# Performance work log

Measured on AMD Instinct MI355X. Metric: run time of the kernel, lower is better.

Reference implementation:

```python
import jax, jax.numpy as jnp
import numpy as np

B, N, F_IN, F_HID, F_EMB, H, L_DIM = 8, 1024, 128, 128, 128, 8, 2


def _xavier(key, shape, fan_in, fan_out):
    lim = np.sqrt(6.0 / (fan_in + fan_out))
    return jax.random.uniform(key, shape, jnp.float32, -lim, lim)


def setup_inputs() -> dict:
    key = jax.random.key(0)
    ks = jax.random.split(key, 16)
    x = jax.random.normal(ks[0], (B, N, F_IN), jnp.float32)
    # sparse 0/1 adjacency with self loops (avoids fully-masked softmax rows)
    adj = (jax.random.uniform(ks[1], (B, N, N)) < 0.05).astype(jnp.float32)
    adj = jnp.maximum(adj, jnp.eye(N, dtype=jnp.float32)[None])
    def gat_params(k, f_in, f_out):
        k1, k2, k3 = jax.random.split(k, 3)
        return (_xavier(k1, (H, f_in, f_out), f_in, f_out),
                _xavier(k2, (H, f_out, 1), f_out, 1),
                _xavier(k3, (H, f_out, 1), f_out, 1),
                jnp.zeros((f_out,), jnp.float32))
    w1, as1, ad1, b1 = gat_params(ks[2], F_IN, F_HID)
    w2, as2, ad2, b2 = gat_params(ks[3], F_HID, F_HID)
    w3, as3, ad3, b3 = gat_params(ks[4], F_HID, F_EMB)
    pred_in = F_HID * 2 + F_EMB  # hidden*(num_layers-1)+embedding, concat=True
    pw = _xavier(ks[5], (pred_in, L_DIM), pred_in, L_DIM)
    pb = jnp.zeros((L_DIM,), jnp.float32)
    return {"x": x, "adj": adj,
            "w1": w1, "as1": as1, "ad1": ad1, "b1": b1,
            "w2": w2, "as2": as2, "ad2": ad2, "b2": b2,
            "w3": w3, "as3": as3, "ad3": ad3, "b3": b3,
            "pw": pw, "pb": pb}


def gat_layer(h, adj, w, a_src, a_dst, bias):
    # h: [B,N,f_in] -> h_prime: [B,H,N,f_out]
    hp = jnp.einsum('bnf,hfo->bhno', h, w)
    t = jnp.tanh(hp)
    s = jnp.einsum('bhno,hoi->bhni', t, a_src)[..., 0]  # [B,H,N]
    d = jnp.einsum('bhno,hoi->bhni', t, a_dst)[..., 0]  # [B,H,N]
    scores = s[:, :, :, None] + d[:, :, None, :]        # [B,H,N,N]
    scores = jnp.where(scores >= 0, scores, 0.2 * scores)  # LeakyReLU(0.2)
    scores = jnp.where(adj[:, None, :, :] > 0, scores, -jnp.inf)
    attn = jax.nn.softmax(scores, axis=-1)  # dropout disabled (eval mode)
    out = jnp.einsum('bhnm,bhmo->bhno', attn, hp) + bias
    return out.mean(axis=1)  # merge heads -> [B,N,f_out]


def reference(x, adj, w1, as1, ad1, b1, w2, as2, ad2, b2, w3, as3, ad3, b3, pw, pb):
    x1 = jax.nn.relu(gat_layer(x, adj, w1, as1, ad1, b1))
    x2 = jax.nn.relu(gat_layer(x1, adj, w2, as2, ad2, b2))
    x3 = gat_layer(x2, adj, w3, as3, ad3, b3)
    x_all = jnp.concatenate([x1, x2, x3], axis=2)  # [B,N,pred_in]
    pooled = jnp.max(x_all, axis=1)                # max over nodes -> [B,pred_in]
    return pooled @ pw + pb                        # [B,label_dim]
```

## Files before the change

kernel.cpp:

```cpp
#include <hip/hip_runtime.h>
#include <hip/hip_fp16.h>

#define BB 8
#define NN 1024
#define FF 128
#define HH 8

typedef _Float16 f16;
typedef f16  f16x8 __attribute__((ext_vector_type(8)));
typedef f16  f16x4 __attribute__((ext_vector_type(4)));
typedef float f32x4 __attribute__((ext_vector_type(4)));

#define L2E 1.44269504f

__global__ void k_pre(const float* __restrict__ x, f16* __restrict__ x16a,
                      const float* __restrict__ w1, const float* __restrict__ w2,
                      const float* __restrict__ w3, f16* __restrict__ wB,
                      const float* __restrict__ adj, unsigned* __restrict__ am){
  int bid = blockIdx.x, t = threadIdx.x;
  if (bid < 512){
    int i = (bid*256 + t)*8;
    float4 a = *(const float4*)(x+i), b = *(const float4*)(x+i+4);
    f16x8 v;
    v[0]=(f16)a.x; v[1]=(f16)a.y; v[2]=(f16)a.z; v[3]=(f16)a.w;
    v[4]=(f16)b.x; v[5]=(f16)b.y; v[6]=(f16)b.z; v[7]=(f16)b.w;
    *(f16x8*)(x16a+i) = v;
  } else if (bid < 704){
    int e = (bid-512)*256 + t;
    int fc = e & 15, c = (e>>4)&127, h = (e>>11)&7, l = e>>14;
    const float* w = (l==0) ? w1 : ((l==1) ? w2 : w3);
    f16x8 v;
    #pragma unroll
    for(int j=0;j<8;j++) v[j] = (f16)w[(h*128 + fc*8 + j)*128 + c];
    *(f16x8*)(wB + (((l*8+h)*16 + fc)*128 + c)*8) = v;
  } else {
    int wv = t >> 6, lane = t & 63;
    int r = (bid-704)*4 + wv;
    const float* row = adj + (long)r*1024;
    for(int g=0; g<16; g++){
      float v = row[g*64 + lane];
      unsigned long long mb = __ballot(v > 0.0f);
      if (lane == 0){
        am[r*32 + 2*g]   = (unsigned)mb;
        am[r*32 + 2*g+1] = (unsigned)(mb >> 32);
      }
    }
  }
}

__global__ __launch_bounds__(256,2) void k_hp(
    const f16* __restrict__ xin,
    const f16* __restrict__ wBl,
    const float* __restrict__ asrc, const float* __restrict__ adst,
    f16* __restrict__ hpB,
    float* __restrict__ sarr, float* __restrict__ darr)
{
  __shared__ f16 xs[128*136];
  __shared__ float asl[128], adl[128];
  int t = threadIdx.x;
  int bid = blockIdx.x;
  int it = bid & 7, h = (bid>>3)&7, b = bid>>6;
  int i0 = it*128;
  {
    const f16* src = xin + (long)(b*1024 + i0)*128;
    int fc = t & 15, r0 = t >> 4;
    #pragma unroll
    for(int p=0;p<8;p++){
      int r = r0 + p*16;
      f16x8 v = *(const f16x8*)(src + r*128 + fc*8);
      *(f16x8*)(xs + r*136 + fc*8) = v;
    }
  }
  if (t < 128){ asl[t] = asrc[h*128+t]; adl[t] = adst[h*128+t]; }
  __syncthreads();

  int lane = t & 63, wv = t>>6, wr = wv>>1, wc = wv&1;
  int mq = lane & 15, quad = lane >> 4;
  f32x4 acc[4][4];
  #pragma unroll
  for(int a=0;a<4;a++)
    #pragma unroll
    for(int c=0;c<4;c++) acc[a][c] = (f32x4){0.f,0.f,0.f,0.f};

  const f16* wh = wBl + h*16*128*8;
  #pragma unroll
  for(int ks=0; ks<4; ks++){
    f16x8 af[4], bf[4];
    #pragma unroll
    for(int mt=0; mt<4; mt++)
      af[mt] = *(const f16x8*)(xs + (wr*64 + mt*16 + mq)*136 + ks*32 + quad*8);
    #pragma unroll
    for(int nt=0; nt<4; nt++){
      int c  = wc*64 + nt*16 + mq;
      int fc = ks*4 + quad;
      bf[nt] = *(const f16x8*)(wh + (fc*128 + c)*8);
    }
    #pragma unroll
    for(int mt=0; mt<4; mt++)
      #pragma unroll
      for(int nt=0; nt<4; nt++)
        acc[mt][nt] = __builtin_amdgcn_mfma_f32_16x16x32_f16(af[mt], bf[nt], acc[mt][nt], 0,0,0);
  }
  __syncthreads();
  f16* tt = xs;
  f16* hpb = hpB + (long)(b*8+h)*128*128*8;
  #pragma unroll
  for(int mt=0; mt<4; mt++){
    #pragma unroll
    for(int nt=0; nt<4; nt++){
      int c = wc*64 + nt*16 + mq;
      f16x4 pk;
      #pragma unroll
      for(int rg=0; rg<4; rg++){
        float v = acc[mt][nt][rg];
        pk[rg] = (f16)v;
        int il = wr*64 + mt*16 + quad*4 + rg;
        float e2 = __expf(2.0f*v);
        float th = 1.0f - 2.0f*__builtin_amdgcn_rcpf(e2 + 1.0f);
        tt[il*136 + c] = (f16)th;
      }
      int il0 = wr*64 + mt*16 + quad*4;
      int inode = i0 + il0;
      *(f16x4*)(hpb + ((long)(inode>>3)*128 + c)*8 + (inode&7)) = pk;
    }
  }
  __syncthreads();
  {
    int r = t>>1, hf = t&1;
    float s_p = 0.f, d_p = 0.f;
    #pragma unroll
    for(int q=0;q<8;q++){
      f16x8 tv = *(const f16x8*)(tt + r*136 + hf*64 + q*8);
      #pragma unroll
      for(int j=0;j<8;j++){
        float tvf = (float)tv[j];
        int c = hf*64 + q*8 + j;
        s_p = fmaf(tvf, asl[c], s_p);
        d_p = fmaf(tvf, adl[c], d_p);
      }
    }
    s_p += __shfl_xor(s_p, 1);
    d_p += __shfl_xor(d_p, 1);
    if (hf == 0){
      sarr[(b*8+h)*1024 + i0 + r] = s_p;
      darr[(b*8+h)*1024 + i0 + r] = d_p;
    }
  }
}

__global__ __launch_bounds__(256,4) void k_attn(
    const f16* __restrict__ hpB,
    const float* __restrict__ sarr, const float* __restrict__ darr,
    const unsigned* __restrict__ am,
    f16* __restrict__ part,
    float* __restrict__ zpart)
{
  __shared__ float ddl[512];
  __shared__ float wred[4];
  __shared__ f16 Pl[2][128*40];
  int t = threadIdx.x;
  int bid = blockIdx.x;
  int bh = bid & 63, q = bid >> 6;
  int jh = q & 1, it = q >> 1;
  int i0 = it*128, j0 = jh*512;
  int b = bh >> 3;

  {
    float4 v = *(const float4*)(darr + bh*1024 + t*4);
    float mx = fmaxf(fmaxf(v.x,v.y), fmaxf(v.z,v.w));
    #pragma unroll
    for(int o=1;o<64;o<<=1) mx = fmaxf(mx, __shfl_xor(mx, o));
    if ((t&63)==0) wred[t>>6] = mx;
    int base = t*4 - j0;
    if (base >= 0 && base < 512){
      float4 s = make_float4(v.x*L2E, v.y*L2E, v.z*L2E, v.w*L2E);
      *(float4*)(ddl + base) = s;
    }
  }
  __syncthreads();
  float Dml = fmaxf(fmaxf(wred[0],wred[1]), fmaxf(wred[2],wred[3])) * L2E;

  int prow = t>>1, pjg = t&1;
  float srowl = sarr[bh*1024 + i0 + prow] * L2E;
  float ml = srowl + Dml;
  float mrowl = fmaxf(ml, 0.2f*ml);
  const unsigned* amrow = am + ((long)(b*1024 + i0 + prow))*32 + jh*16;

  int lane = t&63, wv = t>>6, wr = wv>>1, wc = wv&1;
  int mq = lane&15, quad = lane>>4;
  const f16* hpb = hpB + (long)bh*128*128*8;
  f32x4 acc[4][4];
  #pragma unroll
  for(int a=0;a<4;a++)
    #pragma unroll
    for(int c=0;c<4;c++) acc[a][c] = (f32x4){0.f,0.f,0.f,0.f};
  float zacc = 0.f;
  f16x8 zerov = (f16x8){0,0,0,0,0,0,0,0};

  f16* myp0 = Pl[0] + prow*40 + pjg*16;
  f16* myp1 = Pl[1] + prow*40 + pjg*16;

  auto compP = [&](int jtn, f16* myp){
    *(f16x8*)(myp)     = zerov;
    *(f16x8*)(myp + 8) = zerov;
    unsigned word = (amrow[jtn] >> (pjg*16)) & 0xffffu;
    const float* dloc = ddl + jtn*32 + pjg*16;
    while(word){
      int j = __builtin_ctz(word);
      word &= word - 1u;
      float xl  = srowl + dloc[j];
      float scl = fmaxf(xl, 0.2f*xl);
      float e   = __builtin_amdgcn_exp2f(scl - mrowl);
      zacc += e;
      myp[j] = (f16)e;
    }
  };

  compP(0, myp0);

  #pragma unroll 2
  for(int jt=0; jt<16; jt++){
    f16x8 bf[4];
    #pragma unroll
    for(int nt=0;nt<4;nt++){
      int c  = wc*64 + nt*16 + mq;
      int jc = jh*64 + jt*4 + quad;
      bf[nt] = *(const f16x8*)(hpb + (jc*128 + c)*8);
    }
    __syncthreads();
    const f16* Pb = Pl[jt&1];
    f16x8 af[4];
    #pragma unroll
    for(int mt=0;mt<4;mt++)
      af[mt] = *(const f16x8*)(Pb + (wr*64 + mt*16 + mq)*40 + quad*8);
    if (jt < 15) compP(jt+1, ((jt+1)&1) ? myp1 : myp0);
    #pragma unroll
    for(int mt=0;mt<4;mt++)
      #pragma unroll
      for(int nt=0;nt<4;nt++)
        acc[mt][nt] = __builtin_amdgcn_mfma_f32_16x16x32_f16(af[mt], bf[nt], acc[mt][nt], 0,0,0);
  }
  zacc += __shfl_xor(zacc, 1);
  if (pjg == 0) zpart[(jh*64 + bh)*1024 + i0 + prow] = zacc;
  f16* pout = part + ((long)(jh*64 + bh)*1024 + i0)*128;
  #pragma unroll
  for(int mt=0;mt<4;mt++){
    #pragma unroll
    for(int nt=0;nt<4;nt++){
      int c = wc*64 + nt*16 + mq;
      #pragma unroll
      for(int rg=0;rg<4;rg++){
        int il = wr*64 + mt*16 + quad*4 + rg;
        pout[il*128 + c] = (f16)acc[mt][nt][rg];
      }
    }
  }
}

__global__ void k_fin(const f16* __restrict__ part, const float* __restrict__ zp,
                      const float* __restrict__ bias,
                      f16* __restrict__ x16, float* __restrict__ pmax, int do_relu){
  __shared__ float pm[16][128];
  int t = threadIdx.x;
  int idx = blockIdx.x*256 + t;
  int c8 = idx & 15, n = (idx>>4)&1023, b = idx>>14;
  float s[8];
  #pragma unroll
  for(int j=0;j<8;j++) s[j] = 0.f;
  #pragma unroll
  for(int h=0;h<8;h++){
    int bh = b*8 + h;
    float zi = 0.125f / (zp[bh*1024 + n] + zp[65536 + bh*1024 + n]);
    f16x8 p0 = *(const f16x8*)(part + ((long)bh*1024 + n)*128 + c8*8);
    f16x8 p1 = *(const f16x8*)(part + ((long)(64+bh)*1024 + n)*128 + c8*8);
    #pragma unroll
    for(int j=0;j<8;j++) s[j] = fmaf((float)p0[j] + (float)p1[j], zi, s[j]);
  }
  f16x8 h8;
  float ov[8];
  #pragma unroll
  for(int j=0;j<8;j++){
    float v = s[j] + bias[c8*8 + j];
    if (do_relu) v = fmaxf(v, 0.f);
    ov[j] = v;
    h8[j] = (f16)v;
  }
  if (x16) *(f16x8*)(x16 + ((long)(b*1024+n))*128 + c8*8) = h8;
  #pragma unroll
  for(int j=0;j<8;j++) pm[n&15][c8*8+j] = ov[j];
  __syncthreads();
  if (t < 128){
    float m = pm[0][t];
    #pragma unroll
    for(int r=1;r<16;r++) m = fmaxf(m, pm[r][t]);
    pmax[blockIdx.x*128 + t] = m;
  }
}

__global__ void k_pool2(const float* __restrict__ pmax, const float* __restrict__ pw,
                        const float* __restrict__ pb, float* __restrict__ out){
  __shared__ float pl[384];
  int b = blockIdx.x, t = threadIdx.x;
  for(int f = t; f < 384; f += 256){
    int l = f >> 7, c = f & 127;
    const float* p = pmax + l*65536 + b*64*128 + c;
    float mx = -3.4e38f;
    #pragma unroll 8
    for(int k=0;k<64;k++) mx = fmaxf(mx, p[k*128]);
    pl[f] = mx;
  }
  __syncthreads();
  if (t < 64){
    float a0 = 0.f, a1 = 0.f;
    #pragma unroll
    for(int k=0;k<6;k++){
      int f = t + 64*k;
      float v = pl[f];
      a0 = fmaf(v, pw[f*2],   a0);
      a1 = fmaf(v, pw[f*2+1], a1);
    }
    #pragma unroll
    for(int o=1;o<64;o<<=1){ a0 += __shfl_xor(a0,o); a1 += __shfl_xor(a1,o); }
    if (t == 0){ out[b*2] = a0 + pb[0]; out[b*2+1] = a1 + pb[1]; }
  }
}

extern "C" void kernel_launch(void* const* d_in, const int* in_sizes, int n_in,
                              void* d_out, int out_size, void* d_ws, size_t ws_size,
                              hipStream_t stream) {
  const float* x   = (const float*)d_in[0];
  const float* adj = (const float*)d_in[1];
  const float* w1  = (const float*)d_in[2];
  const float* as1 = (const float*)d_in[3];
  const float* ad1 = (const float*)d_in[4];
  const float* b1  = (const float*)d_in[5];
  const float* w2  = (const float*)d_in[6];
  const float* as2 = (const float*)d_in[7];
  const float* ad2 = (const float*)d_in[8];
  const float* b2  = (const float*)d_in[9];
  const float* w3  = (const float*)d_in[10];
  const float* as3 = (const float*)d_in[11];
  const float* ad3 = (const float*)d_in[12];
  const float* b3  = (const float*)d_in[13];
  const float* pw  = (const float*)d_in[14];
  const float* pb  = (const float*)d_in[15];

  char* ws = (char*)d_ws;
  f16*      x16a = (f16*)ws;                 ws += (size_t)1048576*2;
  f16*      x16b = (f16*)ws;                 ws += (size_t)1048576*2;
  f16*      wB   = (f16*)ws;                 ws += (size_t)393216*2;
  unsigned* am   = (unsigned*)ws;            ws += (size_t)8*1024*32*4;
  f16*      hpB  = (f16*)ws;                 ws += (size_t)8*8*1024*128*2;
  float*    sarr = (float*)ws;               ws += (size_t)65536*4;
  float*    darr = (float*)ws;               ws += (size_t)65536*4;
  f16*      part = (f16*)ws;                 ws += (size_t)2*64*1024*128*2;
  float*    zp   = (float*)ws;               ws += (size_t)2*65536*4;
  float*    pmax = (float*)ws;               ws += (size_t)3*512*128*4;

  k_pre<<<2752, 256, 0, stream>>>(x, x16a, w1, w2, w3, wB, adj, am);

  k_hp  <<<512, 256, 0, stream>>>(x16a, wB,            as1, ad1, hpB, sarr, darr);
  k_attn<<<1024,256, 0, stream>>>(hpB, sarr, darr, am, part, zp);
  k_fin <<<512, 256, 0, stream>>>(part, zp, b1, x16b, pmax,           1);
  k_hp  <<<512, 256, 0, stream>>>(x16b, wB + 131072,   as2, ad2, hpB, sarr, darr);
  k_attn<<<1024,256, 0, stream>>>(hpB, sarr, darr, am, part, zp);
  k_fin <<<512, 256, 0, stream>>>(part, zp, b2, x16a, pmax + 65536,   1);
  k_hp  <<<512, 256, 0, stream>>>(x16a, wB + 262144,   as3, ad3, hpB, sarr, darr);
  k_attn<<<1024,256, 0, stream>>>(hpB, sarr, darr, am, part, zp);
  k_fin <<<512, 256, 0, stream>>>(part, zp, b3, nullptr, pmax + 131072, 0);

  k_pool2<<<8, 256, 0, stream>>>(pmax, pw, pb, (float*)d_out);
}
```

Baseline: 260.0 us.

## Compute attention P tiles branch-free with vectorized loads and prefetched mask words

The sparse per-bit loop (ctz over mask bits with scattered LDS writes plus zeroing) is replaced by a dense, fully unrolled computation of all 16 exponentials, masked with a select and stored as two f16x8 vectors. Adjacency mask words are now prefetched two iterations ahead to hide global load latency. The adjacency read in the mask-building kernel also switches to a nontemporal load. The dense form removes divergent control flow, but it computes exponentials for every entry even though the mask is about 5% dense.

```diff
diff --git a/kernel.cpp b/kernel.cpp
--- a/kernel.cpp
+++ b/kernel.cpp
@@ -38,7 +38,7 @@
     int r = (bid-704)*4 + wv;
     const float* row = adj + (long)r*1024;
     for(int g=0; g<16; g++){
-      float v = row[g*64 + lane];
+      float v = __builtin_nontemporal_load(row + g*64 + lane);
       unsigned long long mb = __ballot(v > 0.0f);
       if (lane == 0){
         am[r*32 + 2*g]   = (unsigned)mb;
@@ -49,11 +49,9 @@
 }
 
 __global__ __launch_bounds__(256,2) void k_hp(
-    const f16* __restrict__ xin,
-    const f16* __restrict__ wBl,
+    const f16* __restrict__ xin, const f16* __restrict__ wBl,
     const float* __restrict__ asrc, const float* __restrict__ adst,
-    f16* __restrict__ hpB,
-    float* __restrict__ sarr, float* __restrict__ darr)
+    f16* __restrict__ hpB, float* __restrict__ sarr, float* __restrict__ darr)
 {
   __shared__ f16 xs[128*136];
   __shared__ float asl[128], adl[128];
@@ -195,28 +193,44 @@
     #pragma unroll
     for(int c=0;c<4;c++) acc[a][c] = (f32x4){0.f,0.f,0.f,0.f};
   float zacc = 0.f;
-  f16x8 zerov = (f16x8){0,0,0,0,0,0,0,0};
 
   f16* myp0 = Pl[0] + prow*40 + pjg*16;
   f16* myp1 = Pl[1] + prow*40 + pjg*16;
 
-  auto compP = [&](int jtn, f16* myp){
-    *(f16x8*)(myp)     = zerov;
-    *(f16x8*)(myp + 8) = zerov;
-    unsigned word = (amrow[jtn] >> (pjg*16)) & 0xffffu;
+  auto compP = [&](int jtn, f16* myp, unsigned w32){
+    unsigned word = (w32 >> (pjg*16)) & 0xffffu;
     const float* dloc = ddl + jtn*32 + pjg*16;
-    while(word){
-      int j = __builtin_ctz(word);
-      word &= word - 1u;
-      float xl  = srowl + dloc[j];
+    float4 dA = *(const float4*)(dloc);
+    float4 dB = *(const float4*)(dloc+4);
+    float dv0[8] = {dA.x,dA.y,dA.z,dA.w, dB.x,dB.y,dB.z,dB.w};
+    f16x8 v;
+    #pragma unroll
+    for(int jj=0;jj<8;jj++){
+      float xl  = srowl + dv0[jj];
       float scl = fmaxf(xl, 0.2f*xl);
       float e   = __builtin_amdgcn_exp2f(scl - mrowl);
+      e = ((word>>jj)&1u) ? e : 0.0f;
       zacc += e;
-      myp[j] = (f16)e;
-    }
+      v[jj] = (f16)e;
+    }
+    *(f16x8*)(myp) = v;
+    float4 dC = *(const float4*)(dloc+8);
+    float4 dD = *(const float4*)(dloc+12);
+    float dv1[8] = {dC.x,dC.y,dC.z,dC.w, dD.x,dD.y,dD.z,dD.w};
+    #pragma unroll
+    for(int jj=0;jj<8;jj++){
+      float xl  = srowl + dv1[jj];
+      float scl = fmaxf(xl, 0.2f*xl);
+      float e   = __builtin_amdgcn_exp2f(scl - mrowl);
+      e = ((word>>(jj+8))&1u) ? e : 0.0f;
+      zacc += e;
+      v[jj] = (f16)e;
+    }
+    *(f16x8*)(myp+8) = v;
   };
 
-  compP(0, myp0);
+  compP(0, myp0, amrow[0]);
+  unsigned wNext = amrow[1];
 
   #pragma unroll 2
   for(int jt=0; jt<16; jt++){
@@ -227,18 +241,20 @@
       int jc = jh*64 + jt*4 + quad;
       bf[nt] = *(const f16x8*)(hpb + (jc*128 + c)*8);
     }
+    unsigned wNN = (jt < 14) ? amrow[jt+2] : 0u;
     __syncthreads();
     const f16* Pb = Pl[jt&1];
     f16x8 af[4];
     #pragma unroll
     for(int mt=0;mt<4;mt++)
       af[mt] = *(const f16x8*)(Pb + (wr*64 + mt*16 + mq)*40 + quad*8);
-    if (jt < 15) compP(jt+1, ((jt+1)&1) ? myp1 : myp0);
+    if (jt < 15) compP(jt+1, ((jt+1)&1) ? myp1 : myp0, wNext);
     #pragma unroll
     for(int mt=0;mt<4;mt++)
       #pragma unroll
       for(int nt=0;nt<4;nt++)
         acc[mt][nt] = __builtin_amdgcn_mfma_f32_16x16x32_f16(af[mt], bf[nt], acc[mt][nt], 0,0,0);
+    wNext = wNN;
   }
   zacc += __shfl_xor(zacc, 1);
   if (pjg == 0) zpart[(jh*64 + bh)*1024 + i0 + prow] = zacc;
```

Result: slower. 288.0 us (+10.8%).
